# Optimization experiments

Hardware: AMD Instinct MI355X
Metric: run time of the kernel (lower is better)

## Reference

```python
import jax, jax.numpy as jnp
import numpy as np

N, G, E, H, Z = 50000, 2000, 800000, 512, 64
BN_EPS = 1e-5


def setup_inputs() -> dict:
    key = jax.random.key(0)
    ks = jax.random.split(key, 10)
    x = jax.random.normal(ks[0], (N, G), dtype=jnp.float32)
    edge_index = jax.random.randint(ks[1], (2, E), 0, N, dtype=jnp.int32)
    s1 = 1.0 / np.sqrt(G)
    s2 = 1.0 / np.sqrt(H)
    return {
        "x": x,
        "edge_index": edge_index,
        "W1l": jax.random.normal(ks[2], (G, H), dtype=jnp.float32) * s1,
        "b1": jnp.zeros((H,), jnp.float32),
        "W1r": jax.random.normal(ks[3], (G, H), dtype=jnp.float32) * s1,
        "bn_gamma": jax.random.uniform(ks[4], (H,), dtype=jnp.float32) + 0.5,
        "bn_beta": jax.random.normal(ks[5], (H,), dtype=jnp.float32) * 0.1,
        "bn_mean": jax.random.normal(ks[6], (H,), dtype=jnp.float32) * 0.1,
        "bn_var": jax.random.uniform(ks[7], (H,), dtype=jnp.float32) + 0.5,
        "W2l": jax.random.normal(ks[8], (H, Z), dtype=jnp.float32) * s2,
        "b2": jnp.zeros((Z,), jnp.float32),
        "W2r": jax.random.normal(ks[9], (H, Z), dtype=jnp.float32) * s2,
    }


def _sage_conv(h, src, dst, Wl, bl, Wr, n_nodes):
    # mean aggregation of source features at destination nodes
    msg = h[src]  # [E, D] gather
    agg = jax.ops.segment_sum(msg, dst, num_segments=n_nodes)
    cnt = jax.ops.segment_sum(jnp.ones((src.shape[0],), h.dtype), dst, num_segments=n_nodes)
    agg = agg / jnp.maximum(cnt, 1.0)[:, None]
    # PyG SAGEConv: lin_l(agg) + lin_r(x), bias only on lin_l
    return agg @ Wl + bl + h @ Wr


def reference(x, edge_index, W1l, b1, W1r, bn_gamma, bn_beta, bn_mean, bn_var, W2l, b2, W2r):
    src, dst = edge_index[0], edge_index[1]
    n = x.shape[0]
    h = _sage_conv(x, src, dst, W1l, b1, W1r, n)  # [N, H]
    # BatchNorm1d (eval mode: running stats) + ReLU; dropout is identity at inference
    h = (h - bn_mean) * (bn_gamma / jnp.sqrt(bn_var + BN_EPS)) + bn_beta
    h = jax.nn.relu(h)
    z = _sage_conv(h, src, dst, W2l, b2, W2r, n)  # [N, Z]
    return z
```

## Files before the change

kernel.cpp:

```cpp
#include <hip/hip_runtime.h>


#define BN_EPS 1e-5f
#define GK 2000
#define KP 2048
#define NKT 32
#define NT2 16

typedef __attribute__((ext_vector_type(8))) short bf16x8;
typedef __attribute__((ext_vector_type(4))) float f32x4;
typedef unsigned short u16x8 __attribute__((ext_vector_type(8)));

__device__ inline unsigned short f2bf(float f) {
    union { float f; unsigned u; } v; v.f = f;
    unsigned r = (v.u + 0x7fffu + ((v.u >> 16) & 1u)) >> 16;
    return (unsigned short)r;
}
__device__ inline float bf2f(unsigned short u) {
    union { unsigned u; float f; } v; v.u = ((unsigned)u) << 16;
    return v.f;
}

#define GLL16(gp, lp) __builtin_amdgcn_global_load_lds( \
    (const __attribute__((address_space(1))) void*)(gp), \
    (__attribute__((address_space(3))) void*)(lp), 16, 0, 0)

__global__ __launch_bounds__(256) void prep2(
    const float* __restrict__ x, unsigned short* __restrict__ xb, int N,
    const float* __restrict__ W1l, const float* __restrict__ W1r,
    const float* __restrict__ gamma, const float* __restrict__ beta,
    const float* __restrict__ mean, const float* __restrict__ var,
    const float* __restrict__ b1, unsigned short* __restrict__ BT,
    const float* __restrict__ W2l, const float* __restrict__ W2r,
    unsigned short* __restrict__ BT2, float* __restrict__ b1p,
    const int* __restrict__ ei, int* __restrict__ cnt, int E)
{
    const int bb = blockIdx.x;
    if (bb < 2048) {
        const int total8 = N * 256;
        for (int idx = bb * 256 + threadIdx.x; idx < total8; idx += 2048 * 256) {
            int row = idx >> 8;
            int k8  = idx & 255;
            unsigned short us[8];
            if (k8 < 250) {
                const float4* p = (const float4*)(x + (size_t)row * 2000 + k8 * 8);
                float4 v0 = p[0], v1 = p[1];
                us[0]=f2bf(v0.x); us[1]=f2bf(v0.y); us[2]=f2bf(v0.z); us[3]=f2bf(v0.w);
                us[4]=f2bf(v1.x); us[5]=f2bf(v1.y); us[6]=f2bf(v1.z); us[7]=f2bf(v1.w);
            } else {
#pragma unroll
                for (int j = 0; j < 8; ++j) us[j] = 0;
            }
            *(u16x8*)&xb[(size_t)row * 2048 + k8 * 8] = *(u16x8*)us;
        }
    } else if (bb < 3072) {
        int idx = (bb - 2048) * 256 + threadIdx.x;
        int c  = idx >> 8;
        int k0 = (idx & 255) << 3;
        int cc = (c < 512) ? c : c - 512;
        float scv = gamma[cc] * rsqrtf(var[cc] + BN_EPS);
        const float* W = (c < 512) ? (W1l + cc) : (W1r + cc);
        unsigned short us[8];
#pragma unroll
        for (int j = 0; j < 8; ++j) {
            int k = k0 + j;
            float v = (k < GK) ? W[(size_t)k * 512] * scv : 0.0f;
            us[j] = f2bf(v);
        }
        *(u16x8*)&BT[(size_t)c * KP + k0] = *(u16x8*)us;
    } else if (bb < 3104) {
        int idx = (bb - 3072) * 256 + threadIdx.x;
        int c  = idx >> 6;
        int k0 = (idx & 63) << 3;
        const float* W = (c < 64) ? (W2l + c) : (W2r + (c - 64));
        unsigned short us[8];
#pragma unroll
        for (int j = 0; j < 8; ++j) us[j] = f2bf(W[(size_t)(k0 + j) * 64]);
        *(u16x8*)&BT2[(size_t)c * 512 + k0] = *(u16x8*)us;
    } else if (bb == 3104) {
#pragma unroll
        for (int h = 0; h < 2; ++h) {
            int c = threadIdx.x + h * 256;
            float scv = gamma[c] * rsqrtf(var[c] + BN_EPS);
            b1p[c] = b1[c] * scv + (beta[c] - mean[c] * scv);
        }
    } else {
        for (int i = (bb - 3105) * 256 + threadIdx.x; i < E; i += 1024 * 256)
            atomicAdd(&cnt[ei[E + i]], 1);
    }
}

__global__ __launch_bounds__(1024) void scan_kernel(const int* __restrict__ cnt,
                                                    int* __restrict__ row_start, int n) {
    __shared__ int part[1024];
    int t = threadIdx.x;
    int chunk = (n + 1023) >> 10;
    int lo = t * chunk;
    int hi = lo + chunk; if (hi > n) hi = n;
    int s = 0;
    for (int i = lo; i < hi; ++i) s += cnt[i];
    part[t] = s;
    __syncthreads();
    for (int off = 1; off < 1024; off <<= 1) {
        int add = (t >= off) ? part[t - off] : 0;
        __syncthreads();
        part[t] += add;
        __syncthreads();
    }
    int run = (t == 0) ? 0 : part[t - 1];
    for (int i = lo; i < hi; ++i) { row_start[i] = run; run += cnt[i]; }
    if (t == 1023) row_start[n] = part[1023];
}

__global__ __launch_bounds__(512) void gemm1_256(
    const unsigned short* __restrict__ xb, int M,
    const unsigned short* __restrict__ BT,
    unsigned short* __restrict__ Y,
    const int* __restrict__ ei, int E, const int* __restrict__ row_start,
    int* __restrict__ cnt, int* __restrict__ colidx)
{
    __shared__ __align__(16) unsigned short As[2][16384];
    __shared__ __align__(16) unsigned short Bs[2][16384];

    const int t = threadIdx.x;
    const int nbr = (M + 255) >> 8;
    const int nwg = nbr * 4;
    const int b   = blockIdx.x;

    if (b >= nwg) {
        int i = (b - nwg) * 512 + t;
        if (i < E) {
            int d = ei[E + i];
            int p = atomicSub(&cnt[d], 1) - 1;
            colidx[row_start[d] + p] = ei[i];
        }
        return;
    }

    const int wid = t >> 6, lane = t & 63;
    int swz = ((nwg & 7) == 0) ? (b & 7) * (nwg >> 3) + (b >> 3) : b;
    const int row0 = (swz >> 2) << 8;
    const int col0 = (swz & 3) << 8;

    const unsigned short* aSrc[4];
    const unsigned short* bSrc[4];
#pragma unroll
    for (int j = 0; j < 4; ++j) {
        int c = t + 512 * j;
        int l = (c & 7) ^ ((c >> 3) & 7);
        int rA = row0 + (c >> 3); if (rA >= M) rA = M - 1;
        aSrc[j] = xb + (size_t)rA * KP + l * 8;
        bSrc[j] = BT + (size_t)(col0 + (c >> 3)) * KP + l * 8;
    }

#define STG_HA0(kt, buf) do { \
        GLL16(aSrc[0] + (size_t)(kt) * 64, &As[buf][(size_t)t * 8]); \
        GLL16(aSrc[1] + (size_t)(kt) * 64, &As[buf][(size_t)(t + 512) * 8]); } while (0)
#define STG_HA1(kt, buf) do { \
        GLL16(aSrc[2] + (size_t)(kt) * 64, &As[buf][(size_t)(1024 + t) * 8]); \
        GLL16(aSrc[3] + (size_t)(kt) * 64, &As[buf][(size_t)(1536 + t) * 8]); } while (0)
#define STG_HB0(kt, buf) do { \
        GLL16(bSrc[0] + (size_t)(kt) * 64, &Bs[buf][(size_t)t * 8]); \
        GLL16(bSrc[1] + (size_t)(kt) * 64, &Bs[buf][(size_t)(t + 512) * 8]); } while (0)
#define STG_HB1(kt, buf) do { \
        GLL16(bSrc[2] + (size_t)(kt) * 64, &Bs[buf][(size_t)(1024 + t) * 8]); \
        GLL16(bSrc[3] + (size_t)(kt) * 64, &Bs[buf][(size_t)(1536 + t) * 8]); } while (0)

    const int wr = wid >> 2, wc = wid & 3;
    const int fr16 = lane & 15;
    const int j4  = lane >> 4;
    const int sl7 = fr16 & 7;
    const int sA0 = ((j4    ) ^ sl7) << 4;
    const int sA1 = ((4 + j4) ^ sl7) << 4;
    const int rbA = (wr * 128 + fr16) << 7;
    const int rbB = (wc * 64  + fr16) << 7;

    f32x4 acc[8][4];
#pragma unroll
    for (int m = 0; m < 8; ++m)
#pragma unroll
        for (int n = 0; n < 4; ++n) acc[m][n] = (f32x4)0.0f;

    STG_HB0(0, 0); STG_HA0(0, 0); STG_HA1(0, 0); STG_HB1(0, 0);
    STG_HB0(1, 1); STG_HA0(1, 1); STG_HA1(1, 1);
    asm volatile("s_waitcnt vmcnt(6)" ::: "memory");
    __builtin_amdgcn_s_barrier();
    __builtin_amdgcn_sched_barrier(0);

    for (int tk = 0; tk < NKT; ++tk) {
        const int buf = tk & 1, obuf = buf ^ 1;
        const char* Ab = (const char*)&As[buf][0];
        const char* Bb = (const char*)&Bs[buf][0];
        bf16x8 af[4][2], bfA[2][2], bfB[2][2];

#pragma unroll
        for (int m = 0; m < 4; ++m) {
            af[m][0] = *(const bf16x8*)(Ab + rbA + (m << 11) + sA0);
            af[m][1] = *(const bf16x8*)(Ab + rbA + (m << 11) + sA1);
        }
#pragma unroll
        for (int n = 0; n < 2; ++n) {
            bfA[n][0] = *(const bf16x8*)(Bb + rbB + (n << 11) + sA0);
            bfA[n][1] = *(const bf16x8*)(Bb + rbB + (n << 11) + sA1);
        }
        STG_HB1(tk + 1, obuf);
        __builtin_amdgcn_s_barrier();
        __builtin_amdgcn_sched_barrier(0);
        __builtin_amdgcn_s_setprio(1);
#pragma unroll
        for (int m = 0; m < 4; ++m)
#pragma unroll
            for (int n = 0; n < 2; ++n) {
                acc[m][n] = __builtin_amdgcn_mfma_f32_16x16x32_bf16(
                    af[m][0], bfA[n][0], acc[m][n], 0, 0, 0);
                acc[m][n] = __builtin_amdgcn_mfma_f32_16x16x32_bf16(
                    af[m][1], bfA[n][1], acc[m][n], 0, 0, 0);
            }
        __builtin_amdgcn_s_setprio(0);

#pragma unroll
        for (int n = 0; n < 2; ++n) {
            bfB[n][0] = *(const bf16x8*)(Bb + rbB + ((n + 2) << 11) + sA0);
            bfB[n][1] = *(const bf16x8*)(Bb + rbB + ((n + 2) << 11) + sA1);
        }
        asm volatile("s_waitcnt lgkmcnt(0)" ::: "memory");
        __builtin_amdgcn_s_barrier();
        __builtin_amdgcn_sched_barrier(0);
        __builtin_amdgcn_s_setprio(1);
#pragma unroll
        for (int m = 0; m < 4; ++m)
#pragma unroll
            for (int n = 0; n < 2; ++n) {
                acc[m][n + 2] = __builtin_amdgcn_mfma_f32_16x16x32_bf16(
                    af[m][0], bfB[n][0], acc[m][n + 2], 0, 0, 0);
                acc[m][n + 2] = __builtin_amdgcn_mfma_f32_16x16x32_bf16(
                    af[m][1], bfB[n][1], acc[m][n + 2], 0, 0, 0);
            }
        __builtin_amdgcn_s_setprio(0);

#pragma unroll
        for (int m = 0; m < 4; ++m) {
            af[m][0] = *(const bf16x8*)(Ab + rbA + ((m + 4) << 11) + sA0);
            af[m][1] = *(const bf16x8*)(Ab + rbA + ((m + 4) << 11) + sA1);
        }
        STG_HB0(tk + 2, buf);
        asm volatile("s_waitcnt lgkmcnt(0)" ::: "memory");
        __builtin_amdgcn_s_barrier();
        __builtin_amdgcn_sched_barrier(0);
        __builtin_amdgcn_s_setprio(1);
#pragma unroll
        for (int m = 0; m < 4; ++m)
#pragma unroll
            for (int n = 0; n < 2; ++n) {
                acc[m + 4][n] = __builtin_amdgcn_mfma_f32_16x16x32_bf16(
                    af[m][0], bfA[n][0], acc[m + 4][n], 0, 0, 0);
                acc[m + 4][n] = __builtin_amdgcn_mfma_f32_16x16x32_bf16(
                    af[m][1], bfA[n][1], acc[m + 4][n], 0, 0, 0);
            }
        __builtin_amdgcn_s_setprio(0);

        STG_HA0(tk + 2, buf);
        STG_HA1(tk + 2, buf);
        asm volatile("s_waitcnt vmcnt(6)" ::: "memory");
        __builtin_amdgcn_s_barrier();
        __builtin_amdgcn_sched_barrier(0);
        __builtin_amdgcn_s_setprio(1);
#pragma unroll
        for (int m = 0; m < 4; ++m)
#pragma unroll
            for (int n = 0; n < 2; ++n) {
                acc[m + 4][n + 2] = __builtin_amdgcn_mfma_f32_16x16x32_bf16(
                    af[m][0], bfB[n][0], acc[m + 4][n + 2], 0, 0, 0);
                acc[m + 4][n + 2] = __builtin_amdgcn_mfma_f32_16x16x32_bf16(
                    af[m][1], bfB[n][1], acc[m + 4][n + 2], 0, 0, 0);
            }
        __builtin_amdgcn_s_setprio(0);
    }
#undef STG_HA0
#undef STG_HA1
#undef STG_HB0
#undef STG_HB1

    const int crow = (lane >> 4) << 2;
#pragma unroll
    for (int m = 0; m < 8; ++m) {
        int rbase = row0 + wr * 128 + m * 16 + crow;
#pragma unroll
        for (int r = 0; r < 4; ++r) {
            int row = rbase + r;
            if (row < M) {
                unsigned short* Yp = Y + (size_t)row * 1024 + col0 + wc * 64 + fr16;
#pragma unroll
                for (int n = 0; n < 4; ++n)
                    Yp[n * 16] = f2bf(acc[m][n][r]);
            }
        }
    }
}

__global__ __launch_bounds__(256) void agg1_kernel(
    const unsigned short* __restrict__ Y, unsigned short* __restrict__ Hh,
    const int* __restrict__ row_start, const int* __restrict__ colidx,
    const float* __restrict__ b1p, int n)
{
    int wid  = (blockIdx.x * blockDim.x + threadIdx.x) >> 6;
    int lane = threadIdx.x & 63;
    if (wid >= n) return;
    int c0 = lane * 8;
    float bb[8];
    *(float4*)&bb[0] = *(const float4*)&b1p[c0];
    *(float4*)&bb[4] = *(const float4*)&b1p[c0 + 4];

    int s0 = row_start[wid], s1 = row_start[wid + 1];
    float acc[8] = {0, 0, 0, 0, 0, 0, 0, 0};
    int i = s0;
    for (; i + 4 <= s1; i += 4) {
        int src0 = colidx[i], src1 = colidx[i + 1];
        int src2 = colidx[i + 2], src3 = colidx[i + 3];
        u16x8 v0 = *(const u16x8*)&Y[(size_t)src0 * 1024 + c0];
        u16x8 v1 = *(const u16x8*)&Y[(size_t)src1 * 1024 + c0];
        u16x8 v2 = *(const u16x8*)&Y[(size_t)src2 * 1024 + c0];
        u16x8 v3 = *(const u16x8*)&Y[(size_t)src3 * 1024 + c0];
#pragma unroll
        for (int j = 0; j < 8; ++j)
            acc[j] += (bf2f(v0[j]) + bf2f(v1[j])) + (bf2f(v2[j]) + bf2f(v3[j]));
    }
    for (; i < s1; ++i) {
        int src = colidx[i];
        u16x8 v = *(const u16x8*)&Y[(size_t)src * 1024 + c0];
#pragma unroll
        for (int j = 0; j < 8; ++j) acc[j] += bf2f(v[j]);
    }
    float inv = 1.0f / fmaxf((float)(s1 - s0), 1.0f);
    u16x8 sv = *(const u16x8*)&Y[(size_t)wid * 1024 + 512 + c0];
    unsigned short o[8];
#pragma unroll
    for (int j = 0; j < 8; ++j) {
        float pre = acc[j] * inv + bb[j] + bf2f(sv[j]);
        o[j] = f2bf(fmaxf(pre, 0.0f));
    }
    *(u16x8*)&Hh[(size_t)wid * 512 + c0] = *(u16x8*)o;
}

__global__ __launch_bounds__(256) void gemm2_bf16(
    const unsigned short* __restrict__ Hh, int M,
    const unsigned short* __restrict__ BT2,
    unsigned short* __restrict__ U)
{
    __shared__ __align__(16) unsigned short As2[2][128][32];
    __shared__ __align__(16) unsigned short Bs2[2][128][32];

    const int t    = threadIdx.x;
    const int wid  = t >> 6;
    const int lane = t & 63;
    const int row0 = blockIdx.x << 7;

    const int c_lo = wid * 64 + lane;
    const int c_hi = c_lo + 256;
    const int s_lo = ((c_lo & 3) ^ ((c_lo >> 3) & 3)) << 3;
    const int s_hi = ((c_hi & 3) ^ ((c_hi >> 3) & 3)) << 3;
    int ra = row0 + (c_lo >> 2); if (ra >= M) ra = M - 1;
    int rbw = row0 + (c_hi >> 2); if (rbw >= M) rbw = M - 1;
    const unsigned short* aSrc0 = Hh + (size_t)ra * 512 + s_lo;
    const unsigned short* aSrc1 = Hh + (size_t)rbw * 512 + s_hi;
    const unsigned short* bSrc0 = BT2 + (size_t)(c_lo >> 2) * 512 + s_lo;
    const unsigned short* bSrc1 = BT2 + (size_t)(c_hi >> 2) * 512 + s_hi;

    const int wr   = wid >> 1, wc = wid & 1;
    const int fr16 = lane & 15;
    const int gsw2 = ((lane >> 4) ^ ((fr16 >> 1) & 3)) << 4;

    f32x4 acc[4][4];
#pragma unroll
    for (int m = 0; m < 4; ++m)
#pragma unroll
        for (int n = 0; n < 4; ++n) acc[m][n] = (f32x4)0.0f;

#define STAGE2(kt, buf) do {                                                  \
        int ko = (kt) * 32;                                                   \
        GLL16(aSrc0 + ko, (unsigned short*)&As2[buf][0][0] + (size_t)c_lo * 8);  \
        GLL16(aSrc1 + ko, (unsigned short*)&As2[buf][0][0] + (size_t)c_hi * 8);  \
        GLL16(bSrc0 + ko, (unsigned short*)&Bs2[buf][0][0] + (size_t)c_lo * 8);  \
        GLL16(bSrc1 + ko, (unsigned short*)&Bs2[buf][0][0] + (size_t)c_hi * 8);  \
    } while (0)

    STAGE2(0, 0);
    int cur = 0;
    for (int it = 0; it < NT2; ++it) {
        __syncthreads();
        if (it + 1 < NT2) STAGE2(it + 1, cur ^ 1);

        const char* Ab = (const char*)&As2[cur][0][0];
        const char* Bb = (const char*)&Bs2[cur][0][0];
        bf16x8 af[4], bfr[4];
#pragma unroll
        for (int m = 0; m < 4; ++m)
            af[m] = *(const bf16x8*)(Ab + ((wr * 64 + m * 16 + fr16) << 6) + gsw2);
#pragma unroll
        for (int n = 0; n < 4; ++n)
            bfr[n] = *(const bf16x8*)(Bb + ((wc * 64 + n * 16 + fr16) << 6) + gsw2);
#pragma unroll
        for (int m = 0; m < 4; ++m)
#pragma unroll
            for (int n = 0; n < 4; ++n)
                acc[m][n] = __builtin_amdgcn_mfma_f32_16x16x32_bf16(
                    af[m], bfr[n], acc[m][n], 0, 0, 0);
        cur ^= 1;
    }
#undef STAGE2

    const int crow = (lane >> 4) << 2;
#pragma unroll
    for (int m = 0; m < 4; ++m) {
        int rbase = row0 + wr * 64 + m * 16 + crow;
#pragma unroll
        for (int r = 0; r < 4; ++r) {
            int row = rbase + r;
            if (row < M) {
                unsigned short* Up = U + (size_t)row * 128 + wc * 64 + fr16;
#pragma unroll
                for (int n = 0; n < 4; ++n)
                    Up[n * 16] = f2bf(acc[m][n][r]);
            }
        }
    }
}

__global__ __launch_bounds__(256) void agg2_kernel(
    const unsigned short* __restrict__ U,
    const int* __restrict__ row_start, const int* __restrict__ colidx,
    const float* __restrict__ b2, float* __restrict__ out, int n)
{
    int wid  = (blockIdx.x * blockDim.x + threadIdx.x) >> 6;
    int lane = threadIdx.x & 63;
    if (wid >= n) return;
    int s0 = row_start[wid], s1 = row_start[wid + 1];
    float acc = 0.f;
    int i = s0;
    for (; i + 4 <= s1; i += 4) {
        int src0 = colidx[i], src1 = colidx[i + 1];
        int src2 = colidx[i + 2], src3 = colidx[i + 3];
        acc += (bf2f(U[(size_t)src0 * 128 + lane]) + bf2f(U[(size_t)src1 * 128 + lane]))
             + (bf2f(U[(size_t)src2 * 128 + lane]) + bf2f(U[(size_t)src3 * 128 + lane]));
    }
    for (; i < s1; ++i) acc += bf2f(U[(size_t)colidx[i] * 128 + lane]);
    float inv = 1.0f / fmaxf((float)(s1 - s0), 1.0f);
    float z = acc * inv + b2[lane] + bf2f(U[(size_t)wid * 128 + 64 + lane]);
    out[(size_t)wid * 64 + lane] = z;
}

extern "C" void kernel_launch(void* const* d_in, const int* in_sizes, int n_in,
                              void* d_out, int out_size, void* d_ws, size_t ws_size,
                              hipStream_t stream) {
    const float* x     = (const float*)d_in[0];
    const int*   ei    = (const int*)d_in[1];
    const float* W1l   = (const float*)d_in[2];
    const float* b1    = (const float*)d_in[3];
    const float* W1r   = (const float*)d_in[4];
    const float* gamma = (const float*)d_in[5];
    const float* beta  = (const float*)d_in[6];
    const float* mean  = (const float*)d_in[7];
    const float* var   = (const float*)d_in[8];
    const float* W2l   = (const float*)d_in[9];
    const float* b2    = (const float*)d_in[10];
    const float* W2r   = (const float*)d_in[11];
    float* out = (float*)d_out;

    const int N = in_sizes[0] / 2000;
    const int E = in_sizes[1] / 2;
    const int nby = (N + 127) / 128;

    char* ws = (char*)d_ws;
    unsigned short* xb  = (unsigned short*)ws;
    unsigned short* Y   = xb + (size_t)N * KP;
    unsigned short* BT  = Y + (size_t)N * 1024;
    unsigned short* BT2 = BT + (size_t)1024 * KP;
    float* b1p     = (float*)(BT2 + (size_t)128 * 512);
    int* cnt       = (int*)(b1p + 512);
    int* row_start = cnt + N;
    int* colidx    = row_start + N + 4;
    unsigned short* Hh = xb;
    unsigned short* U  = Y;

    hipMemsetAsync(cnt, 0, (size_t)N * sizeof(int), stream);

    prep2<<<4129, 256, 0, stream>>>(
        x, xb, N, W1l, W1r, gamma, beta, mean, var, b1, BT,
        W2l, W2r, BT2, b1p, ei, cnt, E);

    scan_kernel<<<1, 1024, 0, stream>>>(cnt, row_start, N);

    int nbr = (N + 255) / 256;
    int nwg = nbr * 4;
    int fillb = (E + 511) / 512;
    gemm1_256<<<nwg + fillb, 512, 0, stream>>>(
        xb, N, BT, Y, ei, E, row_start, cnt, colidx);

    agg1_kernel<<<(N + 3) / 4, 256, 0, stream>>>(
        Y, Hh, row_start, colidx, b1p, N);
    gemm2_bf16<<<nby, 256, 0, stream>>>(Hh, N, BT2, U);
    agg2_kernel<<<(N + 3) / 4, 256, 0, stream>>>(
        U, row_start, colidx, b2, out, N);
}
```

Measured before the change: 654.9 us.

## Fuse layer-1 aggregation into layer-2 GEMM via shared-memory tile

Merges the agg1 gather/mean/ReLU kernel into the second GEMM. Each 128-row block first aggregates its rows into a swizzled 128KB LDS tile, then runs the MFMA loop streaming only the weight tiles. This removes the global write and re-read of the hidden activations and one launch. In exchange the kernel uses about 136KB of LDS, so occupancy is low, and the gather now runs with only 391 blocks of 4 waves, each handling 32 rows serially, which may under-use memory parallelism.

```diff
diff --git a/kernel.cpp b/kernel.cpp
--- a/kernel.cpp
+++ b/kernel.cpp
@@ -298,77 +298,76 @@
     }
 }
 
-__global__ __launch_bounds__(256) void agg1_kernel(
-    const unsigned short* __restrict__ Y, unsigned short* __restrict__ Hh,
+__global__ __launch_bounds__(256) void fused_l2(
+    const unsigned short* __restrict__ Y,
     const int* __restrict__ row_start, const int* __restrict__ colidx,
-    const float* __restrict__ b1p, int n)
+    const float* __restrict__ b1p,
+    const unsigned short* __restrict__ BT2,
+    unsigned short* __restrict__ U, int M)
 {
-    int wid  = (blockIdx.x * blockDim.x + threadIdx.x) >> 6;
-    int lane = threadIdx.x & 63;
-    if (wid >= n) return;
-    int c0 = lane * 8;
-    float bb[8];
-    *(float4*)&bb[0] = *(const float4*)&b1p[c0];
-    *(float4*)&bb[4] = *(const float4*)&b1p[c0 + 4];
-
-    int s0 = row_start[wid], s1 = row_start[wid + 1];
-    float acc[8] = {0, 0, 0, 0, 0, 0, 0, 0};
-    int i = s0;
-    for (; i + 4 <= s1; i += 4) {
-        int src0 = colidx[i], src1 = colidx[i + 1];
-        int src2 = colidx[i + 2], src3 = colidx[i + 3];
-        u16x8 v0 = *(const u16x8*)&Y[(size_t)src0 * 1024 + c0];
-        u16x8 v1 = *(const u16x8*)&Y[(size_t)src1 * 1024 + c0];
-        u16x8 v2 = *(const u16x8*)&Y[(size_t)src2 * 1024 + c0];
-        u16x8 v3 = *(const u16x8*)&Y[(size_t)src3 * 1024 + c0];
-#pragma unroll
-        for (int j = 0; j < 8; ++j)
-            acc[j] += (bf2f(v0[j]) + bf2f(v1[j])) + (bf2f(v2[j]) + bf2f(v3[j]));
-    }
-    for (; i < s1; ++i) {
-        int src = colidx[i];
-        u16x8 v = *(const u16x8*)&Y[(size_t)src * 1024 + c0];
-#pragma unroll
-        for (int j = 0; j < 8; ++j) acc[j] += bf2f(v[j]);
-    }
-    float inv = 1.0f / fmaxf((float)(s1 - s0), 1.0f);
-    u16x8 sv = *(const u16x8*)&Y[(size_t)wid * 1024 + 512 + c0];
-    unsigned short o[8];
-#pragma unroll
-    for (int j = 0; j < 8; ++j) {
-        float pre = acc[j] * inv + bb[j] + bf2f(sv[j]);
-        o[j] = f2bf(fmaxf(pre, 0.0f));
-    }
-    *(u16x8*)&Hh[(size_t)wid * 512 + c0] = *(u16x8*)o;
-}
-
-__global__ __launch_bounds__(256) void gemm2_bf16(
-    const unsigned short* __restrict__ Hh, int M,
-    const unsigned short* __restrict__ BT2,
-    unsigned short* __restrict__ U)
-{
-    __shared__ __align__(16) unsigned short As2[2][128][32];
-    __shared__ __align__(16) unsigned short Bs2[2][128][32];
+    __shared__ __align__(16) unsigned short Ah[128 * 512];
+    __shared__ __align__(16) unsigned short Bs2[2][128 * 32];
 
     const int t    = threadIdx.x;
     const int wid  = t >> 6;
     const int lane = t & 63;
     const int row0 = blockIdx.x << 7;
 
+    {
+        int c0 = lane * 8;
+        float bb[8];
+        *(float4*)&bb[0] = *(const float4*)&b1p[c0];
+        *(float4*)&bb[4] = *(const float4*)&b1p[c0 + 4];
+        for (int rr = wid * 32; rr < wid * 32 + 32; ++rr) {
+            int r = row0 + rr;
+            unsigned short o[8];
+            if (r < M) {
+                int s0 = row_start[r], s1 = row_start[r + 1];
+                float acc[8] = {0, 0, 0, 0, 0, 0, 0, 0};
+                int i = s0;
+                for (; i + 4 <= s1; i += 4) {
+                    int src0 = colidx[i], src1 = colidx[i + 1];
+                    int src2 = colidx[i + 2], src3 = colidx[i + 3];
+                    u16x8 v0 = *(const u16x8*)&Y[(size_t)src0 * 1024 + c0];
+                    u16x8 v1 = *(const u16x8*)&Y[(size_t)src1 * 1024 + c0];
+                    u16x8 v2 = *(const u16x8*)&Y[(size_t)src2 * 1024 + c0];
+                    u16x8 v3 = *(const u16x8*)&Y[(size_t)src3 * 1024 + c0];
+#pragma unroll
+                    for (int j = 0; j < 8; ++j)
+                        acc[j] += (bf2f(v0[j]) + bf2f(v1[j])) + (bf2f(v2[j]) + bf2f(v3[j]));
+                }
+                for (; i < s1; ++i) {
+                    int src = colidx[i];
+                    u16x8 v = *(const u16x8*)&Y[(size_t)src * 1024 + c0];
+#pragma unroll
+                    for (int j = 0; j < 8; ++j) acc[j] += bf2f(v[j]);
+                }
+                float inv = 1.0f / fmaxf((float)(s1 - s0), 1.0f);
+                u16x8 sv = *(const u16x8*)&Y[(size_t)r * 1024 + 512 + c0];
+#pragma unroll
+                for (int j = 0; j < 8; ++j) {
+                    float pre = acc[j] * inv + bb[j] + bf2f(sv[j]);
+                    o[j] = f2bf(fmaxf(pre, 0.0f));
+                }
+            } else {
+#pragma unroll
+                for (int j = 0; j < 8; ++j) o[j] = 0;
+            }
+            *(u16x8*)&Ah[(size_t)rr * 512 + ((lane ^ (rr & 7)) << 3)] = *(u16x8*)o;
+        }
+    }
+
     const int c_lo = wid * 64 + lane;
     const int c_hi = c_lo + 256;
     const int s_lo = ((c_lo & 3) ^ ((c_lo >> 3) & 3)) << 3;
     const int s_hi = ((c_hi & 3) ^ ((c_hi >> 3) & 3)) << 3;
-    int ra = row0 + (c_lo >> 2); if (ra >= M) ra = M - 1;
-    int rbw = row0 + (c_hi >> 2); if (rbw >= M) rbw = M - 1;
-    const unsigned short* aSrc0 = Hh + (size_t)ra * 512 + s_lo;
-    const unsigned short* aSrc1 = Hh + (size_t)rbw * 512 + s_hi;
     const unsigned short* bSrc0 = BT2 + (size_t)(c_lo >> 2) * 512 + s_lo;
     const unsigned short* bSrc1 = BT2 + (size_t)(c_hi >> 2) * 512 + s_hi;
 
     const int wr   = wid >> 1, wc = wid & 1;
     const int fr16 = lane & 15;
-    const int gsw2 = ((lane >> 4) ^ ((fr16 >> 1) & 3)) << 4;
+    const int j4   = lane >> 4;
+    const int gsw2 = (j4 ^ ((fr16 >> 1) & 3)) << 4;
 
     f32x4 acc[4][4];
 #pragma unroll
@@ -376,26 +375,26 @@
 #pragma unroll
         for (int n = 0; n < 4; ++n) acc[m][n] = (f32x4)0.0f;
 
-#define STAGE2(kt, buf) do {                                                  \
-        int ko = (kt) * 32;                                                   \
-        GLL16(aSrc0 + ko, (unsigned short*)&As2[buf][0][0] + (size_t)c_lo * 8);  \
-        GLL16(aSrc1 + ko, (unsigned short*)&As2[buf][0][0] + (size_t)c_hi * 8);  \
-        GLL16(bSrc0 + ko, (unsigned short*)&Bs2[buf][0][0] + (size_t)c_lo * 8);  \
-        GLL16(bSrc1 + ko, (unsigned short*)&Bs2[buf][0][0] + (size_t)c_hi * 8);  \
+#define STAGEB(kt, buf) do {                                           \
+        int ko = (kt) * 32;                                            \
+        GLL16(bSrc0 + ko, &Bs2[buf][(size_t)c_lo * 8]);                \
+        GLL16(bSrc1 + ko, &Bs2[buf][(size_t)c_hi * 8]);                \
     } while (0)
 
-    STAGE2(0, 0);
+    STAGEB(0, 0);
     int cur = 0;
     for (int it = 0; it < NT2; ++it) {
         __syncthreads();
-        if (it + 1 < NT2) STAGE2(it + 1, cur ^ 1);
-
-        const char* Ab = (const char*)&As2[cur][0][0];
-        const char* Bb = (const char*)&Bs2[cur][0][0];
+        if (it + 1 < NT2) STAGEB(it + 1, cur ^ 1);
+
+        const char* Bb = (const char*)&Bs2[cur][0];
         bf16x8 af[4], bfr[4];
 #pragma unroll
-        for (int m = 0; m < 4; ++m)
-            af[m] = *(const bf16x8*)(Ab + ((wr * 64 + m * 16 + fr16) << 6) + gsw2);
+        for (int m = 0; m < 4; ++m) {
+            int rt = wr * 64 + m * 16 + fr16;
+            int slot = (it * 4 + j4) ^ (fr16 & 7);
+            af[m] = *(const bf16x8*)&Ah[(size_t)rt * 512 + (slot << 3)];
+        }
 #pragma unroll
         for (int n = 0; n < 4; ++n)
             bfr[n] = *(const bf16x8*)(Bb + ((wc * 64 + n * 16 + fr16) << 6) + gsw2);
@@ -407,7 +406,7 @@
                     af[m], bfr[n], acc[m][n], 0, 0, 0);
         cur ^= 1;
     }
-#undef STAGE2
+#undef STAGEB
 
     const int crow = (lane >> 4) << 2;
 #pragma unroll
@@ -479,8 +478,7 @@
     int* cnt       = (int*)(b1p + 512);
     int* row_start = cnt + N;
     int* colidx    = row_start + N + 4;
-    unsigned short* Hh = xb;
-    unsigned short* U  = Y;
+    unsigned short* U = xb;
 
     hipMemsetAsync(cnt, 0, (size_t)N * sizeof(int), stream);
 
@@ -496,9 +494,9 @@
     gemm1_256<<<nwg + fillb, 512, 0, stream>>>(
         xb, N, BT, Y, ei, E, row_start, cnt, colidx);
 
-    agg1_kernel<<<(N + 3) / 4, 256, 0, stream>>>(
-        Y, Hh, row_start, colidx, b1p, N);
-    gemm2_bf16<<<nby, 256, 0, stream>>>(Hh, N, BT2, U);
+    fused_l2<<<nby, 256, 0, stream>>>(
+        Y, row_start, colidx, b1p, BT2, U, N);
+
     agg2_kernel<<<(N + 3) / 4, 256, 0, stream>>>(
         U, row_start, colidx, b2, out, N);
 }
```

Measured after the change: 801.5 us. 22.4% more time.
